# Kernel optimization log

Hardware: AMD Instinct MI355X
Metric: run time of the kernel (lower is better)

## Reference

```python
import jax, jax.numpy as jnp
import numpy as np

NUM_PINS = 2_000_000
NUM_PAIRS = 8_000_000


def setup_inputs() -> dict:
    key = jax.random.key(0)
    k1, k2, k3 = jax.random.split(key, 3)
    pin_pos = jax.random.uniform(k1, (2 * NUM_PINS,), dtype=jnp.float32)  # [x...,y...]
    weights = jax.random.uniform(k2, (NUM_PAIRS,), dtype=jnp.float32)
    pairs = jax.random.randint(k3, (2 * NUM_PAIRS,), 0, NUM_PINS, dtype=jnp.int64)
    pin_mask = jnp.zeros((NUM_PINS,), dtype=bool)  # fixed-pin mask (no fixed pins here)
    return {"pin_pos": pin_pos, "weights": weights, "pairs": pairs, "pin_mask": pin_mask}


def reference(pin_pos, weights, pairs, pin_mask):
    num_pins = pin_pos.shape[0] // 2
    x = pin_pos[:num_pins]
    y = pin_pos[num_pins:]
    a = pairs[0::2]  # first pin of each pair
    b = pairs[1::2]  # second pin of each pair
    dx = x[a] - x[b]
    dy = y[a] - y[b]
    # quadratic pin-to-pin attraction energy: sum_i w_i * ||p_a - p_b||^2
    return jnp.sum(weights * (dx * dx + dy * dy))
```

## Files before the change

kernel.cpp:

```cpp
#include <hip/hip_runtime.h>


typedef int   i32x4 __attribute__((ext_vector_type(4)));
typedef float f32x2 __attribute__((ext_vector_type(2)));

__global__ __launch_bounds__(256) void pack_xy_kernel(
    const float* __restrict__ pin_pos,
    f32x2*       __restrict__ xy,
    int num_pins)
{
    const int tid    = blockIdx.x * blockDim.x + threadIdx.x;
    const int stride = gridDim.x * blockDim.x;
    const float* __restrict__ xs = pin_pos;
    const float* __restrict__ ys = pin_pos + num_pins;
    for (int i = tid; i < num_pins; i += stride) {
        f32x2 v;
        v.x = xs[i];
        v.y = ys[i];
        xy[i] = v;
    }
}

__global__ __launch_bounds__(256) void p2p_gather_kernel(
    const f32x2* __restrict__ xy,
    const float* __restrict__ weights,
    const int*   __restrict__ pairs,
    float*       __restrict__ out,
    int num_pairs)
{
    const int tid    = blockIdx.x * blockDim.x + threadIdx.x;
    const int stride = gridDim.x * blockDim.x;

    float acc = 0.0f;

    const i32x4* __restrict__ pairs4 = (const i32x4*)pairs;
    const f32x2* __restrict__ w2     = (const f32x2*)weights;
    const int n2 = num_pairs >> 1;

    for (int i = tid; i < n2; i += stride) {
        i32x4 p = __builtin_nontemporal_load(pairs4 + i);
        f32x2 w = __builtin_nontemporal_load(w2 + i);

        f32x2 A0 = xy[p.x];
        f32x2 B0 = xy[p.y];
        f32x2 A1 = xy[p.z];
        f32x2 B1 = xy[p.w];

        float dx0 = A0.x - B0.x, dy0 = A0.y - B0.y;
        float dx1 = A1.x - B1.x, dy1 = A1.y - B1.y;

        acc += w.x * (dx0 * dx0 + dy0 * dy0);
        acc += w.y * (dx1 * dx1 + dy1 * dy1);
    }

    if ((num_pairs & 1) && tid == 0) {
        int a = pairs[2 * (num_pairs - 1)];
        int b = pairs[2 * (num_pairs - 1) + 1];
        f32x2 A = xy[a], B = xy[b];
        float dx = A.x - B.x, dy = A.y - B.y;
        acc += weights[num_pairs - 1] * (dx * dx + dy * dy);
    }

    for (int off = 32; off > 0; off >>= 1)
        acc += __shfl_down(acc, off, 64);

    __shared__ float wave_sums[4];
    const int lane = threadIdx.x & 63;
    const int wid  = threadIdx.x >> 6;
    if (lane == 0) wave_sums[wid] = acc;
    __syncthreads();

    if (threadIdx.x == 0) {
        float s = wave_sums[0] + wave_sums[1] + wave_sums[2] + wave_sums[3];
        atomicAdd(out, s);
    }
}

__global__ __launch_bounds__(256) void p2p_attraction_fallback(
    const float* __restrict__ pin_pos,
    const float* __restrict__ weights,
    const int*   __restrict__ pairs,
    float*       __restrict__ out,
    int num_pins,
    int num_pairs)
{
    const float* __restrict__ xs = pin_pos;
    const float* __restrict__ ys = pin_pos + num_pins;
    const int tid    = blockIdx.x * blockDim.x + threadIdx.x;
    const int stride = gridDim.x * blockDim.x;
    float acc = 0.0f;
    const i32x4* __restrict__ pairs4 = (const i32x4*)pairs;
    const f32x2* __restrict__ w2     = (const f32x2*)weights;
    const int n2 = num_pairs >> 1;
    for (int i = tid; i < n2; i += stride) {
        i32x4 p = pairs4[i];
        f32x2 w = w2[i];
        float dx0 = xs[p.x] - xs[p.y], dy0 = ys[p.x] - ys[p.y];
        float dx1 = xs[p.z] - xs[p.w], dy1 = ys[p.z] - ys[p.w];
        acc += w.x * (dx0 * dx0 + dy0 * dy0);
        acc += w.y * (dx1 * dx1 + dy1 * dy1);
    }
    if ((num_pairs & 1) && tid == 0) {
        int a = pairs[2 * (num_pairs - 1)];
        int b = pairs[2 * (num_pairs - 1) + 1];
        float dx = xs[a] - xs[b], dy = ys[a] - ys[b];
        acc += weights[num_pairs - 1] * (dx * dx + dy * dy);
    }
    for (int off = 32; off > 0; off >>= 1)
        acc += __shfl_down(acc, off, 64);
    __shared__ float wave_sums[4];
    const int lane = threadIdx.x & 63;
    const int wid  = threadIdx.x >> 6;
    if (lane == 0) wave_sums[wid] = acc;
    __syncthreads();
    if (threadIdx.x == 0) {
        float s = wave_sums[0] + wave_sums[1] + wave_sums[2] + wave_sums[3];
        atomicAdd(out, s);
    }
}

extern "C" void kernel_launch(void* const* d_in, const int* in_sizes, int n_in,
                              void* d_out, int out_size, void* d_ws, size_t ws_size,
                              hipStream_t stream) {
    const float* pin_pos = (const float*)d_in[0];
    const float* weights = (const float*)d_in[1];
    const int*   pairs   = (const int*)d_in[2];

    const int num_pins  = in_sizes[0] / 2;
    const int num_pairs = in_sizes[1];

    float* out = (float*)d_out;

    hipMemsetAsync(out, 0, sizeof(float), stream);

    const int block = 256;
    const int grid  = 2048;

    const size_t xy_bytes = (size_t)num_pins * sizeof(f32x2);
    if (ws_size >= xy_bytes) {
        f32x2* xy = (f32x2*)d_ws;
        pack_xy_kernel<<<grid, block, 0, stream>>>(pin_pos, xy, num_pins);
        p2p_gather_kernel<<<grid, block, 0, stream>>>(
            xy, weights, pairs, out, num_pairs);
    } else {
        p2p_attraction_fallback<<<grid, block, 0, stream>>>(
            pin_pos, weights, pairs, out, num_pins, num_pairs);
    }
}
```

Baseline: 334.0 us.

## Bin pairs by endpoint ranges so each XCD gathers a localized pin subset

Adds a scatter pass that sorts pairs and weights into 64 buckets keyed by the coarse index ranges of both endpoints, using shared-memory histograms and global cursors. A new gather kernel maps each XCD (blockIdx & 7) to the 8 buckets that share one first-endpoint range, so random xy lookups hit a smaller working set in that XCD's L2. Pairs that overflow a bucket's capacity are evaluated directly during the scatter. The cost is an extra read and write of all pair and weight data, shared-memory atomics, and a large workspace requirement; the old path remains as a fallback when the workspace is too small.

```diff
diff --git a/kernel.cpp b/kernel.cpp
--- a/kernel.cpp
+++ b/kernel.cpp
@@ -2,6 +2,7 @@
 
 
 typedef int   i32x4 __attribute__((ext_vector_type(4)));
+typedef int   i32x2 __attribute__((ext_vector_type(2)));
 typedef float f32x2 __attribute__((ext_vector_type(2)));
 
 __global__ __launch_bounds__(256) void pack_xy_kernel(
@@ -14,10 +15,116 @@
     const float* __restrict__ xs = pin_pos;
     const float* __restrict__ ys = pin_pos + num_pins;
     for (int i = tid; i < num_pins; i += stride) {
-        f32x2 v;
-        v.x = xs[i];
-        v.y = ys[i];
+        f32x2 v; v.x = xs[i]; v.y = ys[i];
         xy[i] = v;
+    }
+}
+
+__global__ __launch_bounds__(256) void scatter_bin_kernel(
+    const int*   __restrict__ pairs,
+    const float* __restrict__ weights,
+    const f32x2* __restrict__ xy,
+    i32x2*       __restrict__ ab_out,
+    float*       __restrict__ w_out,
+    int*         __restrict__ cursors,
+    float*       __restrict__ out,
+    int num_pairs, int shift, int cap)
+{
+    const int tid = threadIdx.x;
+    const long start = (long)num_pairs * blockIdx.x / gridDim.x;
+    const long end   = (long)num_pairs * (blockIdx.x + 1) / gridDim.x;
+
+    const i32x2* __restrict__ pr = (const i32x2*)pairs;
+
+    __shared__ int hist[64];
+    __shared__ int base_s[64];
+
+    if (tid < 64) hist[tid] = 0;
+    __syncthreads();
+
+    for (long i = start + tid; i < end; i += 256) {
+        i32x2 p = pr[i];
+        int bin = ((p.x >> shift) << 3) | (p.y >> shift);
+        atomicAdd(&hist[bin], 1);
+    }
+    __syncthreads();
+
+    if (tid < 64) {
+        base_s[tid] = atomicAdd(&cursors[tid], hist[tid]);
+        hist[tid] = 0;
+    }
+    __syncthreads();
+
+    float facc = 0.0f;
+    for (long i = start + tid; i < end; i += 256) {
+        i32x2 p = pr[i];
+        float w = weights[i];
+        int bin = ((p.x >> shift) << 3) | (p.y >> shift);
+        int r = atomicAdd(&hist[bin], 1);
+        long pos = (long)base_s[bin] + r;
+        if (pos < cap) {
+            ab_out[(long)bin * cap + pos] = p;
+            w_out [(long)bin * cap + pos] = w;
+        } else {
+            f32x2 A = xy[p.x], B = xy[p.y];
+            float dx = A.x - B.x, dy = A.y - B.y;
+            facc += w * (dx * dx + dy * dy);
+        }
+    }
+
+    for (int off = 32; off > 0; off >>= 1)
+        facc += __shfl_down(facc, off, 64);
+    __shared__ float wave_sums[4];
+    const int lane = tid & 63, wid = tid >> 6;
+    if (lane == 0) wave_sums[wid] = facc;
+    __syncthreads();
+    if (tid == 0) {
+        float s = wave_sums[0] + wave_sums[1] + wave_sums[2] + wave_sums[3];
+        if (s != 0.0f) atomicAdd(out, s);
+    }
+}
+
+__global__ __launch_bounds__(256) void gather_binned_kernel(
+    const f32x2* __restrict__ xy,
+    const i32x2* __restrict__ ab,
+    const float* __restrict__ wbin,
+    const int*   __restrict__ cursors,
+    float*       __restrict__ out,
+    int cap)
+{
+    const int tid = threadIdx.x;
+    const int xcd = blockIdx.x & 7;
+    const int lb  = blockIdx.x >> 3;
+    const int nlb = gridDim.x >> 3;
+
+    float acc = 0.0f;
+
+    for (int j = 0; j < 8; ++j) {
+        const int bin = xcd * 8 + j;
+        int cnt = cursors[bin];
+        if (cnt > cap) cnt = cap;
+        const int k0 = (int)((long)cnt * lb / nlb);
+        const int k1 = (int)((long)cnt * (lb + 1) / nlb);
+        const i32x2* __restrict__ abp = ab   + (long)bin * cap;
+        const float* __restrict__ wp  = wbin + (long)bin * cap;
+        for (int k = k0 + tid; k < k1; k += 256) {
+            i32x2 p = __builtin_nontemporal_load(abp + k);
+            float w = __builtin_nontemporal_load(wp + k);
+            f32x2 A = xy[p.x], B = xy[p.y];
+            float dx = A.x - B.x, dy = A.y - B.y;
+            acc += w * (dx * dx + dy * dy);
+        }
+    }
+
+    for (int off = 32; off > 0; off >>= 1)
+        acc += __shfl_down(acc, off, 64);
+    __shared__ float wave_sums[4];
+    const int lane = tid & 63, wid = tid >> 6;
+    if (lane == 0) wave_sums[wid] = acc;
+    __syncthreads();
+    if (tid == 0) {
+        float s = wave_sums[0] + wave_sums[1] + wave_sums[2] + wave_sums[3];
+        atomicAdd(out, s);
     }
 }
 
@@ -28,64 +135,6 @@
     float*       __restrict__ out,
     int num_pairs)
 {
-    const int tid    = blockIdx.x * blockDim.x + threadIdx.x;
-    const int stride = gridDim.x * blockDim.x;
-
-    float acc = 0.0f;
-
-    const i32x4* __restrict__ pairs4 = (const i32x4*)pairs;
-    const f32x2* __restrict__ w2     = (const f32x2*)weights;
-    const int n2 = num_pairs >> 1;
-
-    for (int i = tid; i < n2; i += stride) {
-        i32x4 p = __builtin_nontemporal_load(pairs4 + i);
-        f32x2 w = __builtin_nontemporal_load(w2 + i);
-
-        f32x2 A0 = xy[p.x];
-        f32x2 B0 = xy[p.y];
-        f32x2 A1 = xy[p.z];
-        f32x2 B1 = xy[p.w];
-
-        float dx0 = A0.x - B0.x, dy0 = A0.y - B0.y;
-        float dx1 = A1.x - B1.x, dy1 = A1.y - B1.y;
-
-        acc += w.x * (dx0 * dx0 + dy0 * dy0);
-        acc += w.y * (dx1 * dx1 + dy1 * dy1);
-    }
-
-    if ((num_pairs & 1) && tid == 0) {
-        int a = pairs[2 * (num_pairs - 1)];
-        int b = pairs[2 * (num_pairs - 1) + 1];
-        f32x2 A = xy[a], B = xy[b];
-        float dx = A.x - B.x, dy = A.y - B.y;
-        acc += weights[num_pairs - 1] * (dx * dx + dy * dy);
-    }
-
-    for (int off = 32; off > 0; off >>= 1)
-        acc += __shfl_down(acc, off, 64);
-
-    __shared__ float wave_sums[4];
-    const int lane = threadIdx.x & 63;
-    const int wid  = threadIdx.x >> 6;
-    if (lane == 0) wave_sums[wid] = acc;
-    __syncthreads();
-
-    if (threadIdx.x == 0) {
-        float s = wave_sums[0] + wave_sums[1] + wave_sums[2] + wave_sums[3];
-        atomicAdd(out, s);
-    }
-}
-
-__global__ __launch_bounds__(256) void p2p_attraction_fallback(
-    const float* __restrict__ pin_pos,
-    const float* __restrict__ weights,
-    const int*   __restrict__ pairs,
-    float*       __restrict__ out,
-    int num_pins,
-    int num_pairs)
-{
-    const float* __restrict__ xs = pin_pos;
-    const float* __restrict__ ys = pin_pos + num_pins;
     const int tid    = blockIdx.x * blockDim.x + threadIdx.x;
     const int stride = gridDim.x * blockDim.x;
     float acc = 0.0f;
@@ -93,24 +142,55 @@
     const f32x2* __restrict__ w2     = (const f32x2*)weights;
     const int n2 = num_pairs >> 1;
     for (int i = tid; i < n2; i += stride) {
-        i32x4 p = pairs4[i];
-        f32x2 w = w2[i];
-        float dx0 = xs[p.x] - xs[p.y], dy0 = ys[p.x] - ys[p.y];
-        float dx1 = xs[p.z] - xs[p.w], dy1 = ys[p.z] - ys[p.w];
+        i32x4 p = __builtin_nontemporal_load(pairs4 + i);
+        f32x2 w = __builtin_nontemporal_load(w2 + i);
+        f32x2 A0 = xy[p.x], B0 = xy[p.y];
+        f32x2 A1 = xy[p.z], B1 = xy[p.w];
+        float dx0 = A0.x - B0.x, dy0 = A0.y - B0.y;
+        float dx1 = A1.x - B1.x, dy1 = A1.y - B1.y;
         acc += w.x * (dx0 * dx0 + dy0 * dy0);
         acc += w.y * (dx1 * dx1 + dy1 * dy1);
     }
     if ((num_pairs & 1) && tid == 0) {
         int a = pairs[2 * (num_pairs - 1)];
         int b = pairs[2 * (num_pairs - 1) + 1];
+        f32x2 A = xy[a], B = xy[b];
+        float dx = A.x - B.x, dy = A.y - B.y;
+        acc += weights[num_pairs - 1] * (dx * dx + dy * dy);
+    }
+    for (int off = 32; off > 0; off >>= 1)
+        acc += __shfl_down(acc, off, 64);
+    __shared__ float wave_sums[4];
+    const int lane = threadIdx.x & 63, wid = threadIdx.x >> 6;
+    if (lane == 0) wave_sums[wid] = acc;
+    __syncthreads();
+    if (threadIdx.x == 0) {
+        float s = wave_sums[0] + wave_sums[1] + wave_sums[2] + wave_sums[3];
+        atomicAdd(out, s);
+    }
+}
+
+__global__ __launch_bounds__(256) void p2p_direct_kernel(
+    const float* __restrict__ pin_pos,
+    const float* __restrict__ weights,
+    const int*   __restrict__ pairs,
+    float*       __restrict__ out,
+    int num_pins, int num_pairs)
+{
+    const float* __restrict__ xs = pin_pos;
+    const float* __restrict__ ys = pin_pos + num_pins;
+    const int tid    = blockIdx.x * blockDim.x + threadIdx.x;
+    const int stride = gridDim.x * blockDim.x;
+    float acc = 0.0f;
+    for (int i = tid; i < num_pairs; i += stride) {
+        int a = pairs[2 * i], b = pairs[2 * i + 1];
         float dx = xs[a] - xs[b], dy = ys[a] - ys[b];
-        acc += weights[num_pairs - 1] * (dx * dx + dy * dy);
+        acc += weights[i] * (dx * dx + dy * dy);
     }
     for (int off = 32; off > 0; off >>= 1)
         acc += __shfl_down(acc, off, 64);
     __shared__ float wave_sums[4];
-    const int lane = threadIdx.x & 63;
-    const int wid  = threadIdx.x >> 6;
+    const int lane = threadIdx.x & 63, wid = threadIdx.x >> 6;
     if (lane == 0) wave_sums[wid] = acc;
     __syncthreads();
     if (threadIdx.x == 0) {
@@ -130,20 +210,41 @@
     const int num_pairs = in_sizes[1];
 
     float* out = (float*)d_out;
-
     hipMemsetAsync(out, 0, sizeof(float), stream);
 
     const int block = 256;
-    const int grid  = 2048;
+
+    int shift = 0;
+    while (((unsigned)(num_pins - 1) >> shift) > 7u) ++shift;
 
     const size_t xy_bytes = (size_t)num_pins * sizeof(f32x2);
-    if (ws_size >= xy_bytes) {
+    const size_t cur_off  = (xy_bytes + 255) & ~(size_t)255;
+    const size_t ab_off   = cur_off + 256;
+
+    long cap = 0;
+    if (ws_size > ab_off) cap = (long)((ws_size - ab_off) / (64 * 12));
+    if (cap > 250000) cap = 250000;
+
+    if (cap >= 160000) {
+        f32x2* xy      = (f32x2*)d_ws;
+        int*   cursors = (int*)((char*)d_ws + cur_off);
+        i32x2* ab      = (i32x2*)((char*)d_ws + ab_off);
+        float* wbin    = (float*)((char*)d_ws + ab_off + (size_t)64 * cap * sizeof(i32x2));
+
+        hipMemsetAsync(cursors, 0, 64 * sizeof(int), stream);
+        pack_xy_kernel<<<2048, block, 0, stream>>>(pin_pos, xy, num_pins);
+        scatter_bin_kernel<<<1024, block, 0, stream>>>(
+            pairs, weights, xy, ab, wbin, cursors, out,
+            num_pairs, shift, (int)cap);
+        gather_binned_kernel<<<2048, block, 0, stream>>>(
+            xy, ab, wbin, cursors, out, (int)cap);
+    } else if (ws_size >= xy_bytes) {
         f32x2* xy = (f32x2*)d_ws;
-        pack_xy_kernel<<<grid, block, 0, stream>>>(pin_pos, xy, num_pins);
-        p2p_gather_kernel<<<grid, block, 0, stream>>>(
+        pack_xy_kernel<<<2048, block, 0, stream>>>(pin_pos, xy, num_pins);
+        p2p_gather_kernel<<<2048, block, 0, stream>>>(
             xy, weights, pairs, out, num_pairs);
     } else {
-        p2p_attraction_fallback<<<grid, block, 0, stream>>>(
+        p2p_direct_kernel<<<2048, block, 0, stream>>>(
             pin_pos, weights, pairs, out, num_pins, num_pairs);
     }
 }
```

Measured after the change: 416.9 us. 24.8% more time.
